# Kernel tuning notes

Measured on AMD Instinct MI355X. Metric: run time of the kernel, lower is better.

Reference implementation:

```python
import jax, jax.numpy as jnp
import numpy as np

GRID = 64
N = GRID * GRID            # N_NODES = 4096
B = 8
IN_DIM = 12
HID = 64
HEADS = 4
HD = HID                    # per-head channels (GATConv(hidden, hidden, concat=False))
EDGE_DIM = 3
N_ODE_STEPS = 4             # fixed-step RK4 over t in [0, 1] (stands in for dopri5; 16 f-evals)


def _grid_edges():
    """8-neighborhood edges on the 64x64 grid + unit direction vectors."""
    idx = np.arange(N).reshape(GRID, GRID)
    srcs, dsts, dirs = [], [], []
    for dy in (-1, 0, 1):
        for dx in (-1, 0, 1):
            if dy == 0 and dx == 0:
                continue
            r0, r1 = max(0, -dy), GRID - max(0, dy)
            c0, c1 = max(0, -dx), GRID - max(0, dx)
            s = idx[r0:r1, c0:c1].ravel()
            d = idx[r0 + dy:r1 + dy, c0 + dx:c1 + dx].ravel()
            srcs.append(s)
            dsts.append(d)
            v = np.array([dx, dy], dtype=np.float32)
            v /= np.linalg.norm(v)
            dirs.append(np.tile(v, (s.size, 1)))
    edge_index = np.stack([np.concatenate(srcs), np.concatenate(dsts)], 0).astype(np.int32)
    edge_dirs = np.concatenate(dirs, 0).astype(np.float32)
    return jnp.asarray(edge_index), jnp.asarray(edge_dirs)


def _ln(x, g, b):
    m = x.mean(-1, keepdims=True)
    v = x.var(-1, keepdims=True)
    return (x - m) / jnp.sqrt(v + 1e-5) * g + b


def setup_inputs() -> dict:
    key = jax.random.key(0)
    ks = jax.random.split(key, 12)
    edge_index, edge_dirs = _grid_edges()
    x = jax.random.uniform(ks[0], (B, IN_DIM, GRID, GRID), jnp.float32)

    def lin(k, i, o):
        return jax.random.normal(k, (i, o), jnp.float32) / np.sqrt(i)

    return {
        "x": x,
        "edge_index": edge_index,
        "edge_dirs": edge_dirs,
        "W_enc1": lin(ks[1], IN_DIM, HID), "b_enc1": jnp.zeros((HID,), jnp.float32),
        "W_enc2": lin(ks[2], HID, HID), "b_enc2": jnp.zeros((HID,), jnp.float32),
        "W_gat": lin(ks[3], HID, HEADS * HD),
        "att_src": jax.random.normal(ks[4], (HEADS, HD), jnp.float32) / np.sqrt(HD),
        "att_dst": jax.random.normal(ks[5], (HEADS, HD), jnp.float32) / np.sqrt(HD),
        "W_edge": lin(ks[6], EDGE_DIM, HEADS * HD),
        "att_edge": jax.random.normal(ks[7], (HEADS, HD), jnp.float32) / np.sqrt(HD),
        "b_gat": jnp.zeros((HID,), jnp.float32),
        "g_f": jnp.ones((HID,), jnp.float32), "bt_f": jnp.zeros((HID,), jnp.float32),
        "g_h": jnp.ones((HID,), jnp.float32), "bt_h": jnp.zeros((HID,), jnp.float32),
        "W_h1": lin(ks[8], HID, HID), "b_h1": jnp.zeros((HID,), jnp.float32),
        "W_h2": lin(ks[9], HID, 1), "b_h2": jnp.zeros((1,), jnp.float32),
    }


def reference(x, edge_index, edge_dirs, W_enc1, b_enc1, W_enc2, b_enc2, W_gat,
              att_src, att_dst, W_edge, att_edge, b_gat, g_f, bt_f, g_h, bt_h,
              W_h1, b_h1, W_h2, b_h2):
    Bs = x.shape[0]
    E = edge_index.shape[1]
    BN = Bs * N
    nodes = x.reshape(Bs, IN_DIM, N).transpose(0, 2, 1)          # [B, N, 12]
    h = (jax.nn.silu(nodes @ W_enc1 + b_enc1) @ W_enc2 + b_enc2).reshape(BN, HID)

    src, dst = edge_index[0], edge_index[1]
    # edge features: unit direction (2) + fire-channel (ch 0) difference (1)
    diff = nodes[:, dst, 0] - nodes[:, src, 0]                    # [B, E]
    ea = jnp.concatenate(
        [jnp.broadcast_to(edge_dirs[None], (Bs, E, 2)), diff[..., None]], -1
    ).reshape(Bs * E, EDGE_DIM)
    off = (jnp.arange(Bs, dtype=src.dtype) * N)[:, None]
    bsrc = (src[None] + off).reshape(-1)                          # [B*E]
    bdst = (dst[None] + off).reshape(-1)

    # edge-conditioned attention term is constant over ODE time
    e_lin = (ea @ W_edge).reshape(-1, HEADS, HD)                  # [BE, H, C]
    a_edge = (e_lin * att_edge).sum(-1)                           # [BE, H]

    def f(hh):
        xl = (hh @ W_gat).reshape(BN, HEADS, HD)                  # [BN, H, C]
        a_s = (xl * att_src).sum(-1)                              # [BN, H]
        a_d = (xl * att_dst).sum(-1)
        a = jax.nn.leaky_relu(a_s[bsrc] + a_d[bdst] + a_edge, 0.2)
        amax = jax.ops.segment_max(a, bdst, num_segments=BN)      # per-destination softmax
        p = jnp.exp(a - amax[bdst])
        z = jax.ops.segment_sum(p, bdst, num_segments=BN)
        alpha = p / (z[bdst] + 1e-16)                             # [BE, H]
        msg = jax.ops.segment_sum(alpha[:, :, None] * xl[bsrc], bdst, num_segments=BN)
        out = msg.mean(1) + b_gat                                 # heads averaged (concat=False)
        return jax.nn.silu(_ln(out, g_f, bt_f))

    dt = 1.0 / N_ODE_STEPS
    for _ in range(N_ODE_STEPS):                                  # fixed small count: ok
        k1 = f(h)
        k2 = f(h + 0.5 * dt * k1)
        k3 = f(h + 0.5 * dt * k2)
        k4 = f(h + dt * k3)
        h = h + (dt / 6.0) * (k1 + 2.0 * k2 + 2.0 * k3 + k4)

    z = jax.nn.silu(_ln(h, g_h, bt_h) @ W_h1 + b_h1)
    logits = (z @ W_h2 + b_h2).reshape(Bs, GRID, GRID)
    init_fire = x[:, 0]
    logits = jnp.where(init_fire > 0.5, jnp.maximum(logits, 6.0), logits)
    return logits
```

## Files before the change

kernel.cpp:

```cpp
#include <hip/hip_runtime.h>

#define NN 4096
#define BN 32768

typedef __attribute__((ext_vector_type(8))) short short8;
typedef __attribute__((ext_vector_type(4))) float f32x4;

__device__ __forceinline__ float sigmoidf_(float x){ return 1.f/(1.f+__expf(-x)); }
__device__ __forceinline__ unsigned short bfr(float f){
    unsigned int u = __float_as_uint(f);
    u += 0x7FFFu + ((u>>16)&1u);
    return (unsigned short)(u>>16);
}
__device__ __forceinline__ float b2f(unsigned short h){
    return __uint_as_float(((unsigned int)h)<<16);
}

__global__ void prep_kernel(const float* __restrict__ W_gat,
                            const float* __restrict__ att_src,
                            const float* __restrict__ att_dst,
                            const float* __restrict__ W_edge,
                            const float* __restrict__ att_edge,
                            float* __restrict__ As, float* __restrict__ Ad,
                            float* __restrict__ cE,
                            unsigned short* __restrict__ AsAdT,
                            unsigned short* __restrict__ WT2h,
                            unsigned short* __restrict__ WT2l)
{
    int t = threadIdx.x;
    int i = t >> 2, hh = t & 3;
    float s = 0.f, d = 0.f;
    for (int j = 0; j < 64; j++){
        float w = W_gat[i*256 + hh*64 + j];
        s += w * att_src[hh*64 + j];
        d += w * att_dst[hh*64 + j];
    }
    As[t] = s;
    Ad[t] = d;
    if (t < 12){
        int e = t >> 2, h2 = t & 3;
        float cc = 0.f;
        for (int k = 0; k < 64; k++)
            cc += W_edge[e*256 + h2*64 + k] * att_edge[h2*64 + k];
        cE[h2*3 + e] = cc;
    }
    __syncthreads();
    if (t < 16){
        for (int k = 0; k < 64; k++){
            float v = (t < 4) ? As[k*4 + t] : (t < 8 ? Ad[k*4 + (t-4)] : 0.f);
            AsAdT[t*64 + k] = bfr(v);
        }
    }
    {
        int j = t >> 2, q = t & 3;
        for (int k = 0; k < 64; k++){
            float wv = W_gat[k*256 + q*64 + j];
            unsigned short hi = bfr(wv);
            WT2h[j*256 + q*64 + k] = hi;
            WT2l[j*256 + q*64 + k] = bfr(wv - b2f(hi));
        }
    }
}

__global__ __launch_bounds__(256) void enc_kernel(
    const float* __restrict__ x,
    const float* __restrict__ W1, const float* __restrict__ b1,
    const float* __restrict__ W2, const float* __restrict__ b2,
    float* __restrict__ H, float* __restrict__ HA)
{
    __shared__ __align__(16) float sm[5168];
    float* xT  = sm;
    float* t1  = sm + 816;

    int t = threadIdx.x;
    int w = __builtin_amdgcn_readfirstlane(t >> 6);
    int lane = t & 63;
    int n0 = blockIdx.x * 64;
    int b = n0 >> 12;
    int cell0 = n0 & 4095;

    for (int e = t; e < 12*64; e += 256){
        int c = e >> 6, u = e & 63;
        xT[c*68 + u] = x[b*(12*NN) + c*NN + cell0 + u];
    }
    __syncthreads();

    #pragma unroll
    for (int jj = 0; jj < 16; jj++){
        int j = w*16 + jj;
        float a = b1[j];
        #pragma unroll
        for (int c = 0; c < 12; c++)
            a += xT[c*68 + lane] * W1[c*64 + j];
        t1[j*68 + lane] = a * sigmoidf_(a);
    }
    __syncthreads();

    float hk[16];
    #pragma unroll
    for (int kk = 0; kk < 16; kk++) hk[kk] = b2[w*16 + kk];
    for (int j = 0; j < 64; j++){
        float v = t1[j*68 + lane];
        #pragma unroll
        for (int kk = 0; kk < 16; kk++)
            hk[kk] += v * W2[j*64 + w*16 + kk];
    }
    int hb = (n0 + lane)*64 + w*16;
    #pragma unroll
    for (int j4 = 0; j4 < 4; j4++){
        float4 v = make_float4(hk[4*j4+0], hk[4*j4+1], hk[4*j4+2], hk[4*j4+3]);
        *(float4*)&H[hb + 4*j4]  = v;
        *(float4*)&HA[hb + 4*j4] = v;
    }
}

__global__ __launch_bounds__(256) void f_kernel(
    const float* __restrict__ HINc,
    const float* __restrict__ x,
    const float* __restrict__ CCE,
    const unsigned short* __restrict__ AsAdT,
    const unsigned short* __restrict__ WT2h, const unsigned short* __restrict__ WT2l,
    const float* __restrict__ b_gat, const float* __restrict__ g_f, const float* __restrict__ bt_f,
    float* __restrict__ H, float* __restrict__ HOUT, float* __restrict__ ACC,
    int stage)
{
    __shared__ __align__(16) char smem[29376];
    unsigned short* hA = (unsigned short*)smem;
    float* aL  = (float*)(smem + 16128);
    float* as2 = (float*)(smem + 25344);
    float* ad2 = (float*)(smem + 27136);
    float* x0h = (float*)(smem + 28928);

    int t = threadIdx.x;
    int w = __builtin_amdgcn_readfirstlane(t >> 6);
    int lane = t & 63;
    int l15 = lane & 15, lg = lane >> 4;
    int blk = blockIdx.x;
    int b = blk & 7, tile = blk >> 3;
    int tr = tile >> 3, tc = tile & 7;
    int r0 = tr*8 - 1, c0 = tc*8 - 1;
    int nb = b*NN;
    int xb = b*(12*NN);

    const int DYI[8] = {-1,-1,-1,0,0,1,1,1};
    const int DXI[8] = {-1,0,1,-1,1,-1,0,1};
    const float s2c = 0.70710678f;
    const float DXN[8] = {-s2c,0.f,s2c,-1.f,1.f,-s2c,0.f,s2c};
    const float DYN[8] = {-s2c,-1.f,-s2c,0.f,0.f,s2c,1.f,s2c};

    for (int u = t; u < 432; u += 256)
        ((unsigned int*)(smem + 14400))[u] = 0u;
    for (int u = t; u < 1600; u += 256){
        int m = u >> 4, k4 = u & 15;
        int hr = m/10, hc = m - hr*10;
        int r = min(63,max(0,r0+hr)), c = min(63,max(0,c0+hc));
        float4 v = *(const float4*)&HINc[(long)(nb + r*64 + c)*64 + k4*4];
        unsigned int p0 = (unsigned int)bfr(v.x) | ((unsigned int)bfr(v.y)<<16);
        unsigned int p1 = (unsigned int)bfr(v.z) | ((unsigned int)bfr(v.w)<<16);
        *(uint2*)&hA[m*72 + k4*4] = make_uint2(p0,p1);
        if (k4 == 0) x0h[m] = x[xb + r*64 + c];
    }
    __syncthreads();

    for (int nt = w; nt < 7; nt += 4){
        f32x4 acc = {0.f,0.f,0.f,0.f};
        #pragma unroll
        for (int kt = 0; kt < 2; kt++){
            short8 afr  = *(const short8*)&AsAdT[l15*64 + kt*32 + lg*8];
            short8 bfrg = *(const short8*)&hA[(nt*16+l15)*72 + kt*32 + lg*8];
            acc = __builtin_amdgcn_mfma_f32_16x16x32_bf16(afr, bfrg, acc, 0,0,0);
        }
        int m = nt*16 + l15;
        if (lg == 0)      *(float4*)&as2[m*4] = make_float4(acc[0],acc[1],acc[2],acc[3]);
        else if (lg == 1) *(float4*)&ad2[m*4] = make_float4(acc[0],acc[1],acc[2],acc[3]);
    }
    __syncthreads();

    {
        int e = lane;
        int er = e >> 3, ec = e & 7;
        int gr = tr*8 + er, gc = tc*8 + ec;
        int me = (er+1)*10 + (ec+1);
        float adv = ad2[me*4 + w];
        float x0n = x0h[me];
        float ce0 = CCE[w*3+0], ce1 = CCE[w*3+1], ce2 = CCE[w*3+2];
        float al[8]; float mx = -1e30f;
        #pragma unroll
        for (int o = 0; o < 8; o++){
            int mr = gr - DYI[o], mc = gc - DXI[o];
            bool vld = (mr>=0)&&(mr<64)&&(mc>=0)&&(mc<64);
            int hm = me - DYI[o]*10 - DXI[o];
            float a = as2[hm*4+w] + adv + ce0*DXN[o] + ce1*DYN[o]
                    + ce2*(x0n - x0h[hm]);
            a = (a >= 0.f) ? a : 0.2f*a;
            al[o] = vld ? a : -1e30f;
            mx = fmaxf(mx, al[o]);
        }
        float z = 0.f;
        #pragma unroll
        for (int o = 0; o < 8; o++){
            float p = (al[o] > -1e29f) ? __expf(al[o]-mx) : 0.f;
            al[o] = p; z += p;
        }
        float zi = 1.f/(z + 1e-16f);
        #pragma unroll
        for (int o = 0; o < 8; o++)
            aL[e*36 + o*4 + w] = al[o]*zi;
    }
    __syncthreads();

    int e2 = w*16 + l15;
    int er2 = e2 >> 3, ec2 = e2 & 7;
    int me2 = (er2+1)*10 + (ec2+1);
    float G[8][8];
    #pragma unroll
    for (int kt = 0; kt < 8; kt++)
        #pragma unroll
        for (int i = 0; i < 8; i++) G[kt][i] = 0.f;
    #pragma unroll
    for (int o = 0; o < 8; o++){
        int hm = me2 - DYI[o]*10 - DXI[o];
        float4 ao = *(const float4*)&aL[e2*36 + o*4];
        const unsigned short* hp = &hA[hm*72 + lg*8];
        short8 v0 = *(const short8*)&hp[0];
        short8 v1 = *(const short8*)&hp[32];
        #pragma unroll
        for (int i = 0; i < 8; i++){
            float f0 = b2f((unsigned short)v0[i]);
            float f1 = b2f((unsigned short)v1[i]);
            G[0][i] += ao.x*f0;  G[1][i] += ao.x*f1;
            G[2][i] += ao.y*f0;  G[3][i] += ao.y*f1;
            G[4][i] += ao.z*f0;  G[5][i] += ao.z*f1;
            G[6][i] += ao.w*f0;  G[7][i] += ao.w*f1;
        }
    }

    f32x4 oacc[4];
    #pragma unroll
    for (int nt = 0; nt < 4; nt++) oacc[nt] = (f32x4){0.f,0.f,0.f,0.f};
    #pragma unroll
    for (int kt = 0; kt < 8; kt++){
        short8 afr;
        #pragma unroll
        for (int i = 0; i < 8; i++) afr[i] = (short)bfr(G[kt][i]);
        #pragma unroll
        for (int nt = 0; nt < 4; nt++){
            short8 bh = *(const short8*)&WT2h[(nt*16+l15)*256 + kt*32 + lg*8];
            oacc[nt] = __builtin_amdgcn_mfma_f32_16x16x32_bf16(afr, bh, oacc[nt], 0,0,0);
        }
        #pragma unroll
        for (int nt = 0; nt < 4; nt++){
            short8 bl = *(const short8*)&WT2l[(nt*16+l15)*256 + kt*32 + lg*8];
            oacc[nt] = __builtin_amdgcn_mfma_f32_16x16x32_bf16(afr, bl, oacc[nt], 0,0,0);
        }
    }

    float bg[4], gf[4], bf_[4];
    #pragma unroll
    for (int nt = 0; nt < 4; nt++){
        int j = nt*16 + l15;
        bg[nt] = b_gat[j]; gf[nt] = g_f[j]; bf_[nt] = bt_f[j];
    }
    #pragma unroll
    for (int reg = 0; reg < 4; reg++){
        int e3 = w*16 + lg*4 + reg;
        float vv[4];
        float s1 = 0.f, s2 = 0.f;
        #pragma unroll
        for (int nt = 0; nt < 4; nt++){
            float v = oacc[nt][reg]*0.25f + bg[nt];
            vv[nt] = v; s1 += v; s2 += v*v;
        }
        s1 += __shfl_xor(s1,1); s2 += __shfl_xor(s2,1);
        s1 += __shfl_xor(s1,2); s2 += __shfl_xor(s2,2);
        s1 += __shfl_xor(s1,4); s2 += __shfl_xor(s2,4);
        s1 += __shfl_xor(s1,8); s2 += __shfl_xor(s2,8);
        float mean = s1*(1.f/64.f);
        float var  = s2*(1.f/64.f) - mean*mean;
        float rstd = rsqrtf(fmaxf(var,0.f) + 1e-5f);
        int r2 = e3 >> 3, c2 = e3 & 7;
        long gn = nb + (tr*8 + r2)*64 + (tc*8 + c2);
        #pragma unroll
        for (int nt = 0; nt < 4; nt++){
            int j = nt*16 + l15;
            float y = (vv[nt]-mean)*rstd*gf[nt] + bf_[nt];
            float kv = y * sigmoidf_(y);
            long idx = gn*64 + j;
            float hold = H[idx];
            float hn;
            if (stage == 0){
                ACC[idx] = kv;                 hn = hold + 0.125f*kv;
            } else if (stage == 1){
                ACC[idx] += 2.f*kv;            hn = hold + 0.125f*kv;
            } else if (stage == 2){
                ACC[idx] += 2.f*kv;            hn = hold + 0.25f*kv;
            } else {
                hn = hold + (0.25f/6.f)*(ACC[idx] + kv);
                H[idx] = hn;
            }
            HOUT[idx] = hn;
        }
    }
}

__global__ __launch_bounds__(256) void head_kernel(
    const float* __restrict__ H, const float* __restrict__ x,
    const float* __restrict__ g_h, const float* __restrict__ bt_h,
    const float* __restrict__ Wh1, const float* __restrict__ bh1,
    const float* __restrict__ Wh2, const float* __restrict__ bh2,
    float* __restrict__ out)
{
    __shared__ __align__(16) float sm[4624];
    float* hT = sm;
    float* pl = sm + 4352;

    int t = threadIdx.x;
    int w = __builtin_amdgcn_readfirstlane(t >> 6);
    int lane = t & 63;
    int n0 = blockIdx.x * 64;
    int b = n0 >> 12;
    int cell0 = n0 & 4095;

    for (int e = t; e < 4096; e += 256){
        int n = e >> 6, j = e & 63;
        hT[j*68 + n] = H[(n0+n)*64 + j];
    }
    __syncthreads();

    float s1 = 0.f, s2 = 0.f;
    for (int j = 0; j < 64; j++){
        float v = hT[j*68 + lane];
        s1 += v; s2 += v*v;
    }
    float mean = s1*(1.f/64.f);
    float var  = s2*(1.f/64.f) - mean*mean;
    float rstd = rsqrtf(fmaxf(var, 0.f) + 1e-5f);

    float acc[16];
    #pragma unroll
    for (int kk = 0; kk < 16; kk++) acc[kk] = bh1[w*16 + kk];
    for (int j = 0; j < 64; j++){
        float v = (hT[j*68 + lane] - mean)*rstd*g_h[j] + bt_h[j];
        #pragma unroll
        for (int kk = 0; kk < 16; kk++)
            acc[kk] += v * Wh1[j*64 + w*16 + kk];
    }
    float plg = 0.f;
    #pragma unroll
    for (int kk = 0; kk < 16; kk++){
        float a = acc[kk];
        plg += (a * sigmoidf_(a)) * Wh2[w*16 + kk];
    }
    pl[w*68 + lane] = plg;
    __syncthreads();
    if (t < 64){
        float lgt = pl[0*68+t] + pl[1*68+t] + pl[2*68+t] + pl[3*68+t] + bh2[0];
        float fire = x[b*(12*NN) + cell0 + t];
        out[n0 + t] = (fire > 0.5f) ? fmaxf(lgt, 6.f) : lgt;
    }
}

extern "C" void kernel_launch(void* const* d_in, const int* in_sizes, int n_in,
                              void* d_out, int out_size, void* d_ws, size_t ws_size,
                              hipStream_t stream)
{
    const float* x       = (const float*)d_in[0];
    const float* W_enc1  = (const float*)d_in[3];
    const float* b_enc1  = (const float*)d_in[4];
    const float* W_enc2  = (const float*)d_in[5];
    const float* b_enc2  = (const float*)d_in[6];
    const float* W_gat   = (const float*)d_in[7];
    const float* att_src = (const float*)d_in[8];
    const float* att_dst = (const float*)d_in[9];
    const float* W_edge  = (const float*)d_in[10];
    const float* att_edge= (const float*)d_in[11];
    const float* b_gat   = (const float*)d_in[12];
    const float* g_f     = (const float*)d_in[13];
    const float* bt_f    = (const float*)d_in[14];
    const float* g_h     = (const float*)d_in[15];
    const float* bt_h    = (const float*)d_in[16];
    const float* W_h1    = (const float*)d_in[17];
    const float* b_h1    = (const float*)d_in[18];
    const float* W_h2    = (const float*)d_in[19];
    const float* b_h2    = (const float*)d_in[20];

    float* ws  = (float*)d_ws;
    float* H   = ws;
    float* HA  = ws + 2097152;
    float* HB  = ws + 4194304;
    float* ACC = ws + 6291456;
    float* CAS = ws + 8388608;
    float* CAD = ws + 8388864;
    float* CCE = ws + 8389120;
    unsigned short* AsAdT = (unsigned short*)(ws + 8389376);
    unsigned short* WT2h  = (unsigned short*)(ws + 8389888);
    unsigned short* WT2l  = (unsigned short*)(ws + 8398080);
    float* out = (float*)d_out;

    prep_kernel<<<1, 256, 0, stream>>>(W_gat, att_src, att_dst, W_edge, att_edge,
                                       CAS, CAD, CCE, AsAdT, WT2h, WT2l);
    enc_kernel<<<512, 256, 0, stream>>>(x, W_enc1, b_enc1, W_enc2, b_enc2, H, HA);

    float* hin = HA; float* hout = HB;
    for (int step = 0; step < 4; step++){
        for (int st = 0; st < 4; st++){
            f_kernel<<<512, 256, 0, stream>>>(hin, x, CCE, AsAdT, WT2h, WT2l,
                                              b_gat, g_f, bt_f,
                                              H, hout, ACC, st);
            float* tm = hin; hin = hout; hout = tm;
        }
    }

    head_kernel<<<512, 256, 0, stream>>>(H, x, g_h, bt_h, W_h1, b_h1, W_h2, b_h2, out);
}
```

Baseline: 512.6 us.

## Store intermediate ODE state as bf16 and split f_kernel across 8 waves

The stage input buffers between RK4 evaluations are now stored as bf16 instead of fp32, which halves the halo-load traffic in f_kernel and removes the per-load conversion. The f_kernel block grows to 512 threads. The head-split aggregation and output projection are divided between two wave groups, each handling two heads, and partial results are reduced through a new shared-memory buffer. This adds a barrier and leaves half the waves idle in the epilogue, in exchange for more parallelism per block and fewer registers (G array halved). Stored values are rounded to bf16 as before, so numerics are unchanged.

Result: slower. 734.0 us (+43.2%).

```diff
diff --git a/kernel.cpp b/kernel.cpp
--- a/kernel.cpp
+++ b/kernel.cpp
@@ -66,7 +66,7 @@
     const float* __restrict__ x,
     const float* __restrict__ W1, const float* __restrict__ b1,
     const float* __restrict__ W2, const float* __restrict__ b2,
-    float* __restrict__ H, float* __restrict__ HA)
+    float* __restrict__ H, unsigned short* __restrict__ HX)
 {
     __shared__ __align__(16) float sm[5168];
     float* xT  = sm;
@@ -107,32 +107,35 @@
     }
     int hb = (n0 + lane)*64 + w*16;
     #pragma unroll
-    for (int j4 = 0; j4 < 4; j4++){
-        float4 v = make_float4(hk[4*j4+0], hk[4*j4+1], hk[4*j4+2], hk[4*j4+3]);
-        *(float4*)&H[hb + 4*j4]  = v;
-        *(float4*)&HA[hb + 4*j4] = v;
-    }
-}
-
-__global__ __launch_bounds__(256) void f_kernel(
-    const float* __restrict__ HINc,
+    for (int j4 = 0; j4 < 4; j4++)
+        *(float4*)&H[hb + 4*j4] = make_float4(hk[4*j4+0], hk[4*j4+1], hk[4*j4+2], hk[4*j4+3]);
+    unsigned int* dst = (unsigned int*)&HX[hb];
+    #pragma unroll
+    for (int p = 0; p < 8; p++)
+        dst[p] = (unsigned int)bfr(hk[2*p]) | ((unsigned int)bfr(hk[2*p+1])<<16);
+}
+
+__global__ __launch_bounds__(512, 4) void f_kernel(
+    const unsigned short* __restrict__ HIN,
     const float* __restrict__ x,
     const float* __restrict__ CCE,
     const unsigned short* __restrict__ AsAdT,
     const unsigned short* __restrict__ WT2h, const unsigned short* __restrict__ WT2l,
     const float* __restrict__ b_gat, const float* __restrict__ g_f, const float* __restrict__ bt_f,
-    float* __restrict__ H, float* __restrict__ HOUT, float* __restrict__ ACC,
+    float* __restrict__ H, unsigned short* __restrict__ HOUT, float* __restrict__ ACC,
     int stage)
 {
-    __shared__ __align__(16) char smem[29376];
+    __shared__ __align__(16) char smem[46784];
     unsigned short* hA = (unsigned short*)smem;
-    float* aL  = (float*)(smem + 16128);
-    float* as2 = (float*)(smem + 25344);
-    float* ad2 = (float*)(smem + 27136);
-    float* x0h = (float*)(smem + 28928);
+    float* aL   = (float*)(smem + 16128);
+    float* as2  = (float*)(smem + 25344);
+    float* ad2  = (float*)(smem + 27136);
+    float* x0h  = (float*)(smem + 28928);
+    float* osum = (float*)(smem + 29376);
 
     int t = threadIdx.x;
     int w = __builtin_amdgcn_readfirstlane(t >> 6);
+    int rt = w & 3, hp = w >> 2;
     int lane = t & 63;
     int l15 = lane & 15, lg = lane >> 4;
     int blk = blockIdx.x;
@@ -148,49 +151,54 @@
     const float DXN[8] = {-s2c,0.f,s2c,-1.f,1.f,-s2c,0.f,s2c};
     const float DYN[8] = {-s2c,-1.f,-s2c,0.f,0.f,s2c,1.f,s2c};
 
-    for (int u = t; u < 432; u += 256)
-        ((unsigned int*)(smem + 14400))[u] = 0u;
-    for (int u = t; u < 1600; u += 256){
-        int m = u >> 4, k4 = u & 15;
+    for (int u = t; u < 800; u += 512){
+        int m = u >> 3, k8 = u & 7;
         int hr = m/10, hc = m - hr*10;
         int r = min(63,max(0,r0+hr)), c = min(63,max(0,c0+hc));
-        float4 v = *(const float4*)&HINc[(long)(nb + r*64 + c)*64 + k4*4];
-        unsigned int p0 = (unsigned int)bfr(v.x) | ((unsigned int)bfr(v.y)<<16);
-        unsigned int p1 = (unsigned int)bfr(v.z) | ((unsigned int)bfr(v.w)<<16);
-        *(uint2*)&hA[m*72 + k4*4] = make_uint2(p0,p1);
-        if (k4 == 0) x0h[m] = x[xb + r*64 + c];
-    }
-    __syncthreads();
-
-    for (int nt = w; nt < 7; nt += 4){
+        *(uint4*)&hA[m*72 + k8*8] = *(const uint4*)&HIN[(long)(nb + r*64 + c)*64 + k8*8];
+    }
+    for (int u = t; u < 432; u += 512)
+        ((unsigned int*)(smem + 14400))[u] = 0u;
+    if (t < 112){
+        float v = 0.f;
+        if (t < 100){
+            int hr = t/10, hc = t - hr*10;
+            int r = min(63,max(0,r0+hr)), c = min(63,max(0,c0+hc));
+            v = x[xb + r*64 + c];
+        }
+        x0h[t] = v;
+    }
+    __syncthreads();
+
+    if (w < 7){
         f32x4 acc = {0.f,0.f,0.f,0.f};
         #pragma unroll
         for (int kt = 0; kt < 2; kt++){
             short8 afr  = *(const short8*)&AsAdT[l15*64 + kt*32 + lg*8];
-            short8 bfrg = *(const short8*)&hA[(nt*16+l15)*72 + kt*32 + lg*8];
+            short8 bfrg = *(const short8*)&hA[(w*16+l15)*72 + kt*32 + lg*8];
             acc = __builtin_amdgcn_mfma_f32_16x16x32_bf16(afr, bfrg, acc, 0,0,0);
         }
-        int m = nt*16 + l15;
+        int m = w*16 + l15;
         if (lg == 0)      *(float4*)&as2[m*4] = make_float4(acc[0],acc[1],acc[2],acc[3]);
         else if (lg == 1) *(float4*)&ad2[m*4] = make_float4(acc[0],acc[1],acc[2],acc[3]);
     }
     __syncthreads();
 
-    {
-        int e = lane;
+    if (t < 256){
+        int e = t & 63, hh = t >> 6;
         int er = e >> 3, ec = e & 7;
         int gr = tr*8 + er, gc = tc*8 + ec;
         int me = (er+1)*10 + (ec+1);
-        float adv = ad2[me*4 + w];
+        float adv = ad2[me*4 + hh];
         float x0n = x0h[me];
-        float ce0 = CCE[w*3+0], ce1 = CCE[w*3+1], ce2 = CCE[w*3+2];
+        float ce0 = CCE[hh*3+0], ce1 = CCE[hh*3+1], ce2 = CCE[hh*3+2];
         float al[8]; float mx = -1e30f;
         #pragma unroll
         for (int o = 0; o < 8; o++){
             int mr = gr - DYI[o], mc = gc - DXI[o];
             bool vld = (mr>=0)&&(mr<64)&&(mc>=0)&&(mc<64);
             int hm = me - DYI[o]*10 - DXI[o];
-            float a = as2[hm*4+w] + adv + ce0*DXN[o] + ce1*DYN[o]
+            float a = as2[hm*4+hh] + adv + ce0*DXN[o] + ce1*DYN[o]
                     + ce2*(x0n - x0h[hm]);
             a = (a >= 0.f) ? a : 0.2f*a;
             al[o] = vld ? a : -1e30f;
@@ -205,33 +213,30 @@
         float zi = 1.f/(z + 1e-16f);
         #pragma unroll
         for (int o = 0; o < 8; o++)
-            aL[e*36 + o*4 + w] = al[o]*zi;
-    }
-    __syncthreads();
-
-    int e2 = w*16 + l15;
-    int er2 = e2 >> 3, ec2 = e2 & 7;
-    int me2 = (er2+1)*10 + (ec2+1);
-    float G[8][8];
-    #pragma unroll
-    for (int kt = 0; kt < 8; kt++)
+            aL[e*36 + o*4 + hh] = al[o]*zi;
+    }
+    __syncthreads();
+
+    int e2 = rt*16 + l15;
+    int me2 = ((e2>>3)+1)*10 + ((e2&7)+1);
+    float G[4][8];
+    #pragma unroll
+    for (int kt = 0; kt < 4; kt++)
         #pragma unroll
         for (int i = 0; i < 8; i++) G[kt][i] = 0.f;
     #pragma unroll
     for (int o = 0; o < 8; o++){
         int hm = me2 - DYI[o]*10 - DXI[o];
-        float4 ao = *(const float4*)&aL[e2*36 + o*4];
-        const unsigned short* hp = &hA[hm*72 + lg*8];
-        short8 v0 = *(const short8*)&hp[0];
-        short8 v1 = *(const short8*)&hp[32];
+        float2 ao = *(const float2*)&aL[e2*36 + o*4 + hp*2];
+        const unsigned short* hp8 = &hA[hm*72 + lg*8];
+        short8 v0 = *(const short8*)&hp8[0];
+        short8 v1 = *(const short8*)&hp8[32];
         #pragma unroll
         for (int i = 0; i < 8; i++){
             float f0 = b2f((unsigned short)v0[i]);
             float f1 = b2f((unsigned short)v1[i]);
             G[0][i] += ao.x*f0;  G[1][i] += ao.x*f1;
             G[2][i] += ao.y*f0;  G[3][i] += ao.y*f1;
-            G[4][i] += ao.z*f0;  G[5][i] += ao.z*f1;
-            G[6][i] += ao.w*f0;  G[7][i] += ao.w*f1;
         }
     }
 
@@ -239,66 +244,77 @@
     #pragma unroll
     for (int nt = 0; nt < 4; nt++) oacc[nt] = (f32x4){0.f,0.f,0.f,0.f};
     #pragma unroll
-    for (int kt = 0; kt < 8; kt++){
+    for (int ktl = 0; ktl < 4; ktl++){
         short8 afr;
         #pragma unroll
-        for (int i = 0; i < 8; i++) afr[i] = (short)bfr(G[kt][i]);
+        for (int i = 0; i < 8; i++) afr[i] = (short)bfr(G[ktl][i]);
+        int kcol = (hp*4 + ktl)*32 + lg*8;
         #pragma unroll
         for (int nt = 0; nt < 4; nt++){
-            short8 bh = *(const short8*)&WT2h[(nt*16+l15)*256 + kt*32 + lg*8];
+            short8 bh = *(const short8*)&WT2h[(nt*16+l15)*256 + kcol];
             oacc[nt] = __builtin_amdgcn_mfma_f32_16x16x32_bf16(afr, bh, oacc[nt], 0,0,0);
         }
         #pragma unroll
         for (int nt = 0; nt < 4; nt++){
-            short8 bl = *(const short8*)&WT2l[(nt*16+l15)*256 + kt*32 + lg*8];
+            short8 bl = *(const short8*)&WT2l[(nt*16+l15)*256 + kcol];
             oacc[nt] = __builtin_amdgcn_mfma_f32_16x16x32_bf16(afr, bl, oacc[nt], 0,0,0);
         }
     }
 
-    float bg[4], gf[4], bf_[4];
-    #pragma unroll
-    for (int nt = 0; nt < 4; nt++){
-        int j = nt*16 + l15;
-        bg[nt] = b_gat[j]; gf[nt] = g_f[j]; bf_[nt] = bt_f[j];
-    }
-    #pragma unroll
-    for (int reg = 0; reg < 4; reg++){
-        int e3 = w*16 + lg*4 + reg;
-        float vv[4];
-        float s1 = 0.f, s2 = 0.f;
-        #pragma unroll
-        for (int nt = 0; nt < 4; nt++){
-            float v = oacc[nt][reg]*0.25f + bg[nt];
-            vv[nt] = v; s1 += v; s2 += v*v;
-        }
-        s1 += __shfl_xor(s1,1); s2 += __shfl_xor(s2,1);
-        s1 += __shfl_xor(s1,2); s2 += __shfl_xor(s2,2);
-        s1 += __shfl_xor(s1,4); s2 += __shfl_xor(s2,4);
-        s1 += __shfl_xor(s1,8); s2 += __shfl_xor(s2,8);
-        float mean = s1*(1.f/64.f);
-        float var  = s2*(1.f/64.f) - mean*mean;
-        float rstd = rsqrtf(fmaxf(var,0.f) + 1e-5f);
-        int r2 = e3 >> 3, c2 = e3 & 7;
-        long gn = nb + (tr*8 + r2)*64 + (tc*8 + c2);
+    if (hp == 0){
+        #pragma unroll
+        for (int nt = 0; nt < 4; nt++)
+            #pragma unroll
+            for (int reg = 0; reg < 4; reg++)
+                osum[(rt*16 + lg*4 + reg)*68 + nt*16 + l15] = oacc[nt][reg];
+    }
+    __syncthreads();
+
+    if (hp == 1){
+        float bg[4], gf[4], bf_[4];
         #pragma unroll
         for (int nt = 0; nt < 4; nt++){
             int j = nt*16 + l15;
-            float y = (vv[nt]-mean)*rstd*gf[nt] + bf_[nt];
-            float kv = y * sigmoidf_(y);
-            long idx = gn*64 + j;
-            float hold = H[idx];
-            float hn;
-            if (stage == 0){
-                ACC[idx] = kv;                 hn = hold + 0.125f*kv;
-            } else if (stage == 1){
-                ACC[idx] += 2.f*kv;            hn = hold + 0.125f*kv;
-            } else if (stage == 2){
-                ACC[idx] += 2.f*kv;            hn = hold + 0.25f*kv;
-            } else {
-                hn = hold + (0.25f/6.f)*(ACC[idx] + kv);
-                H[idx] = hn;
+            bg[nt] = b_gat[j]; gf[nt] = g_f[j]; bf_[nt] = bt_f[j];
+        }
+        #pragma unroll
+        for (int reg = 0; reg < 4; reg++){
+            int e3 = rt*16 + lg*4 + reg;
+            float vv[4];
+            float s1 = 0.f, s2 = 0.f;
+            #pragma unroll
+            for (int nt = 0; nt < 4; nt++){
+                float v = (oacc[nt][reg] + osum[e3*68 + nt*16 + l15])*0.25f + bg[nt];
+                vv[nt] = v; s1 += v; s2 += v*v;
             }
-            HOUT[idx] = hn;
+            s1 += __shfl_xor(s1,1); s2 += __shfl_xor(s2,1);
+            s1 += __shfl_xor(s1,2); s2 += __shfl_xor(s2,2);
+            s1 += __shfl_xor(s1,4); s2 += __shfl_xor(s2,4);
+            s1 += __shfl_xor(s1,8); s2 += __shfl_xor(s2,8);
+            float mean = s1*(1.f/64.f);
+            float var  = s2*(1.f/64.f) - mean*mean;
+            float rstd = rsqrtf(fmaxf(var,0.f) + 1e-5f);
+            long gn = nb + (tr*8 + (e3>>3))*64 + tc*8 + (e3&7);
+            #pragma unroll
+            for (int nt = 0; nt < 4; nt++){
+                int j = nt*16 + l15;
+                float y = (vv[nt]-mean)*rstd*gf[nt] + bf_[nt];
+                float kv = y * sigmoidf_(y);
+                long idx = gn*64 + j;
+                float hold = H[idx];
+                float hn;
+                if (stage == 0){
+                    ACC[idx] = kv;                 hn = hold + 0.125f*kv;
+                } else if (stage == 1){
+                    ACC[idx] += 2.f*kv;            hn = hold + 0.125f*kv;
+                } else if (stage == 2){
+                    ACC[idx] += 2.f*kv;            hn = hold + 0.25f*kv;
+                } else {
+                    hn = hold + (0.25f/6.f)*(ACC[idx] + kv);
+                    H[idx] = hn;
+                }
+                HOUT[idx] = bfr(hn);
+            }
         }
     }
 }
@@ -386,28 +402,28 @@
 
     float* ws  = (float*)d_ws;
     float* H   = ws;
-    float* HA  = ws + 2097152;
-    float* HB  = ws + 4194304;
-    float* ACC = ws + 6291456;
-    float* CAS = ws + 8388608;
-    float* CAD = ws + 8388864;
-    float* CCE = ws + 8389120;
-    unsigned short* AsAdT = (unsigned short*)(ws + 8389376);
-    unsigned short* WT2h  = (unsigned short*)(ws + 8389888);
-    unsigned short* WT2l  = (unsigned short*)(ws + 8398080);
+    float* ACC = ws + 2097152;
+    float* CAS = ws + 4194304;
+    float* CAD = ws + 4194560;
+    float* CCE = ws + 4194816;
+    unsigned short* AsAdT = (unsigned short*)(ws + 4195072);
+    unsigned short* WT2h  = (unsigned short*)(ws + 4195584);
+    unsigned short* WT2l  = (unsigned short*)(ws + 4203776);
+    unsigned short* HXA   = (unsigned short*)(ws + 4211968);
+    unsigned short* HXB   = (unsigned short*)(ws + 4736256);
     float* out = (float*)d_out;
 
     prep_kernel<<<1, 256, 0, stream>>>(W_gat, att_src, att_dst, W_edge, att_edge,
                                        CAS, CAD, CCE, AsAdT, WT2h, WT2l);
-    enc_kernel<<<512, 256, 0, stream>>>(x, W_enc1, b_enc1, W_enc2, b_enc2, H, HA);
-
-    float* hin = HA; float* hout = HB;
+    enc_kernel<<<512, 256, 0, stream>>>(x, W_enc1, b_enc1, W_enc2, b_enc2, H, HXA);
+
+    unsigned short* hin = HXA; unsigned short* hout = HXB;
     for (int step = 0; step < 4; step++){
         for (int st = 0; st < 4; st++){
-            f_kernel<<<512, 256, 0, stream>>>(hin, x, CCE, AsAdT, WT2h, WT2l,
+            f_kernel<<<512, 512, 0, stream>>>(hin, x, CCE, AsAdT, WT2h, WT2l,
                                               b_gat, g_f, bt_f,
                                               H, hout, ACC, st);
-            float* tm = hin; hin = hout; hout = tm;
+            unsigned short* tm = hin; hin = hout; hout = tm;
         }
     }
 
```
